# Optimization experiments

Hardware: AMD Instinct MI355X
Metric: run time of the kernel (lower is better)

Reference implementation:

```python
import jax, jax.numpy as jnp
import numpy as np

HEADS, DIM_HEAD, LANDMARKS, PINV_ITERS = 8, 64, 256, 6
DIM = 512
KERNEL = 33  # residual depthwise conv kernel size (lucidrains NystromAttention default)
EPS = 1e-5   # torch LayerNorm eps


def setup_inputs() -> dict:
    key = jax.random.key(0)
    ks = jax.random.split(key, 4)
    b, n = 4, 8192  # n divisible by LANDMARKS -> no padding branch
    w = lambda k, shape: jax.random.normal(k, shape, dtype=jnp.float32) * 0.02
    return {
        "x": jax.random.normal(ks[0], (b, n, DIM), dtype=jnp.float32),
        "ln_gamma": jnp.ones((DIM,), jnp.float32),
        "ln_beta": jnp.zeros((DIM,), jnp.float32),
        "w_qkv": w(ks[1], (DIM, 3 * HEADS * DIM_HEAD)),   # to_qkv, no bias
        "w_out": w(ks[2], (HEADS * DIM_HEAD, DIM)),
        "b_out": jnp.zeros((DIM,), jnp.float32),
        "res_kernel": w(ks[3], (HEADS, 1, KERNEL, 1)),    # Conv2d(heads, heads, (33,1), groups=heads)
    }


def _moore_penrose_pinv(a, iters):
    # iterative Moore-Penrose pseudoinverse (lucidrains)
    abs_a = jnp.abs(a)
    col = abs_a.sum(-1).max()  # global max, matching torch.max(col)
    row = abs_a.sum(-2).max()
    z = jnp.swapaxes(a, -1, -2) / (col * row)
    I = jnp.eye(a.shape[-1], dtype=a.dtype)
    for _ in range(iters):
        az = a @ z
        z = 0.25 * z @ (13.0 * I - az @ (15.0 * I - az @ (7.0 * I - az)))
    return z


def reference(x, ln_gamma, ln_beta, w_qkv, w_out, b_out, res_kernel):
    b, n, d = x.shape
    h, dh, m = HEADS, DIM_HEAD, LANDMARKS
    # --- LayerNorm ---
    mu = x.mean(-1, keepdims=True)
    var = ((x - mu) ** 2).mean(-1, keepdims=True)
    xn = (x - mu) * jax.lax.rsqrt(var + EPS) * ln_gamma + ln_beta
    # --- qkv projection ---
    qkv = xn @ w_qkv                                   # (b, n, 3*h*dh)
    q, k, v = jnp.split(qkv, 3, axis=-1)
    to_heads = lambda t: t.reshape(b, n, h, dh).transpose(0, 2, 1, 3)  # (b, h, n, dh)
    q, k, v = to_heads(q), to_heads(k), to_heads(v)
    q = q * (dh ** -0.5)
    # --- landmark pooling (mean over groups of l tokens) ---
    l = n // m
    q_l = q.reshape(b, h, m, l, dh).mean(3)            # (b, h, m, dh)
    k_l = k.reshape(b, h, m, l, dh).mean(3)
    # --- three similarity matrices + softmaxes ---
    attn1 = jax.nn.softmax(jnp.einsum('bhnd,bhmd->bhnm', q, k_l), axis=-1)    # (b,h,n,m)
    attn2 = jax.nn.softmax(jnp.einsum('bhid,bhjd->bhij', q_l, k_l), axis=-1)  # (b,h,m,m)
    attn3 = jax.nn.softmax(jnp.einsum('bhmd,bhnd->bhmn', q_l, k), axis=-1)    # (b,h,m,n)
    out = (attn1 @ _moore_penrose_pinv(attn2, PINV_ITERS)) @ (attn3 @ v)      # (b,h,n,dh)
    # --- depthwise residual conv over sequence dim (groups = heads) ---
    res = jax.lax.conv_general_dilated(
        v, res_kernel, window_strides=(1, 1),
        padding=((KERNEL // 2, KERNEL // 2), (0, 0)),
        dimension_numbers=('NCHW', 'OIHW', 'NCHW'),
        feature_group_count=h)
    out = out + res
    # --- merge heads, output projection, outer residual ---
    out = out.transpose(0, 2, 1, 3).reshape(b, n, h * dh)
    att = out @ w_out + b_out
    return x + att
```

## Files before the change

### kernel.cpp

```cpp
#include <hip/hip_runtime.h>
#include <math.h>

#define NB 4
#define NSEQ 8192
#define DMODEL 512
#define NHEADS 8
#define DHEAD 64
#define NLM 256
#define LTOK 32
#define NBH 32
#define KCONV 33
#define CH3 8

typedef unsigned short bf16_t;
typedef __attribute__((ext_vector_type(8))) short bf16x8;
typedef __attribute__((ext_vector_type(4))) float f32x4;

__device__ __forceinline__ float bf2f(bf16_t u) {
  return __uint_as_float(((unsigned)u) << 16);
}
__device__ __forceinline__ bf16_t f2bf(float f) {
  unsigned u = __float_as_uint(f);
  return (bf16_t)((u + 0x7fffu + ((u >> 16) & 1u)) >> 16);
}
__device__ __forceinline__ void bfpair(unsigned u, float& lo, float& hi) {
  lo = __uint_as_float(u << 16);
  hi = __uint_as_float(u & 0xffff0000u);
}
__device__ __forceinline__ void gload16(const bf16_t* g, bf16_t* l) {
  __builtin_amdgcn_global_load_lds(
      (const __attribute__((address_space(1))) unsigned int*)g,
      (__attribute__((address_space(3))) unsigned int*)l, 16, 0, 0);
}

__global__ __launch_bounds__(256) void ln_kernel(const float* __restrict__ x,
    const float* __restrict__ gamma, const float* __restrict__ beta,
    bf16_t* __restrict__ xn) {
  int row = blockIdx.x * 4 + (threadIdx.x >> 6);
  int lane = threadIdx.x & 63;
  const float4* xr = reinterpret_cast<const float4*>(x + (size_t)row * DMODEL);
  float4 a0 = xr[lane];
  float4 a1 = xr[lane + 64];
  float s  = a0.x + a0.y + a0.z + a0.w + a1.x + a1.y + a1.z + a1.w;
  float s2 = a0.x*a0.x + a0.y*a0.y + a0.z*a0.z + a0.w*a0.w
           + a1.x*a1.x + a1.y*a1.y + a1.z*a1.z + a1.w*a1.w;
  #pragma unroll
  for (int off = 32; off; off >>= 1) {
    s  += __shfl_down(s, off);
    s2 += __shfl_down(s2, off);
  }
  s = __shfl(s, 0); s2 = __shfl(s2, 0);
  float mu = s * (1.0f / DMODEL);
  float var = s2 * (1.0f / DMODEL) - mu * mu;
  float rs = rsqrtf(var + 1e-5f);
  const float4* g4 = reinterpret_cast<const float4*>(gamma);
  const float4* b4 = reinterpret_cast<const float4*>(beta);
  float4 g0 = g4[lane], g1 = g4[lane + 64];
  float4 bb0 = b4[lane], bb1 = b4[lane + 64];
  ushort4 o0, o1;
  o0.x = f2bf((a0.x - mu) * rs * g0.x + bb0.x);
  o0.y = f2bf((a0.y - mu) * rs * g0.y + bb0.y);
  o0.z = f2bf((a0.z - mu) * rs * g0.z + bb0.z);
  o0.w = f2bf((a0.w - mu) * rs * g0.w + bb0.w);
  o1.x = f2bf((a1.x - mu) * rs * g1.x + bb1.x);
  o1.y = f2bf((a1.y - mu) * rs * g1.y + bb1.y);
  o1.z = f2bf((a1.z - mu) * rs * g1.z + bb1.z);
  o1.w = f2bf((a1.w - mu) * rs * g1.w + bb1.w);
  ushort4* o = reinterpret_cast<ushort4*>(xn + (size_t)row * DMODEL);
  o[lane] = o0; o[lane + 64] = o1;
}

__global__ void castT2_kernel(const float* __restrict__ wqkv, const float* __restrict__ wout,
                              bf16_t* __restrict__ wqkvT, bf16_t* __restrict__ woutT) {
  int idx = blockIdx.x * 256 + threadIdx.x;
  if (idx < 786432) {
    int k = idx & 511, c = idx >> 9;
    float v = wqkv[(size_t)k * 1536 + c];
    if (c < 512) v *= 0.125f;
    wqkvT[idx] = f2bf(v);
  } else {
    int i = idx - 786432;
    int k = i & 511, c = i >> 9;
    woutT[i] = f2bf(wout[(size_t)k * 512 + c]);
  }
}

__global__ __launch_bounds__(256) void gemm_qkv_mfma(const bf16_t* __restrict__ A,
    const bf16_t* __restrict__ Bt, bf16_t* __restrict__ q, bf16_t* __restrict__ k,
    bf16_t* __restrict__ v) {
  __shared__ __align__(16) bf16_t As[128 * 32];
  __shared__ __align__(16) bf16_t Bs[128 * 32];
  int rowB = blockIdx.x * 128, colB = blockIdx.y * 128;
  int tid = threadIdx.x;
  int wave = tid >> 6, lane = tid & 63;
  int wr = (wave >> 1) * 64, wc = (wave & 1) * 64;
  int lrow = lane & 15, g = lane >> 4;
  f32x4 acc[4][4] = {};
  for (int k0 = 0; k0 < DMODEL; k0 += 32) {
    #pragma unroll
    for (int c = 0; c < 2; ++c) {
      int eb = wave * 1024 + c * 512;
      int e = eb + lane * 8;
      int r = e >> 5, cc = e & 31;
      gload16(A + (size_t)(rowB + r) * DMODEL + k0 + cc, &As[eb]);
      gload16(Bt + (size_t)(colB + r) * DMODEL + k0 + cc, &Bs[eb]);
    }
    __syncthreads();
    bf16x8 af[4], bf[4];
    #pragma unroll
    for (int m = 0; m < 4; ++m)
      af[m] = *reinterpret_cast<const bf16x8*>(&As[(wr + m * 16 + lrow) * 32 + g * 8]);
    #pragma unroll
    for (int n = 0; n < 4; ++n)
      bf[n] = *reinterpret_cast<const bf16x8*>(&Bs[(wc + n * 16 + lrow) * 32 + g * 8]);
    #pragma unroll
    for (int m = 0; m < 4; ++m)
      #pragma unroll
      for (int n = 0; n < 4; ++n)
        acc[m][n] = __builtin_amdgcn_mfma_f32_16x16x32_bf16(af[m], bf[n], acc[m][n], 0, 0, 0);
    __syncthreads();
  }
  #pragma unroll
  for (int m = 0; m < 4; ++m) {
    #pragma unroll
    for (int n = 0; n < 4; ++n) {
      int col = colB + wc + n * 16 + lrow;
      int which = col >> 9, hc = col & 511, h = hc >> 6, d = hc & 63;
      bf16_t* dst = (which == 0) ? q : (which == 1 ? k : v);
      #pragma unroll
      for (int r = 0; r < 4; ++r) {
        int row = rowB + wr + m * 16 + g * 4 + r;
        int b = row >> 13, nn = row & 8191;
        dst[((size_t)(b * NHEADS + h) * NSEQ + nn) * DHEAD + d] = f2bf(acc[m][n][r]);
      }
    }
  }
}

__global__ __launch_bounds__(256) void gemm_out_mfma(const bf16_t* __restrict__ A,
    const bf16_t* __restrict__ Bt, const float* __restrict__ bo,
    const float* __restrict__ x, float* __restrict__ y) {
  __shared__ __align__(16) bf16_t As[128 * 32];
  __shared__ __align__(16) bf16_t Bs[128 * 32];
  int rowB = blockIdx.x * 128, colB = blockIdx.y * 128;
  int tid = threadIdx.x;
  int wave = tid >> 6, lane = tid & 63;
  int wr = (wave >> 1) * 64, wc = (wave & 1) * 64;
  int lrow = lane & 15, g = lane >> 4;
  f32x4 acc[4][4] = {};
  for (int k0 = 0; k0 < DMODEL; k0 += 32) {
    #pragma unroll
    for (int c = 0; c < 2; ++c) {
      int eb = wave * 1024 + c * 512;
      int e = eb + lane * 8;
      int r = e >> 5, cc = e & 31;
      gload16(A + (size_t)(rowB + r) * DMODEL + k0 + cc, &As[eb]);
      gload16(Bt + (size_t)(colB + r) * DMODEL + k0 + cc, &Bs[eb]);
    }
    __syncthreads();
    bf16x8 af[4], bf[4];
    #pragma unroll
    for (int m = 0; m < 4; ++m)
      af[m] = *reinterpret_cast<const bf16x8*>(&As[(wr + m * 16 + lrow) * 32 + g * 8]);
    #pragma unroll
    for (int n = 0; n < 4; ++n)
      bf[n] = *reinterpret_cast<const bf16x8*>(&Bs[(wc + n * 16 + lrow) * 32 + g * 8]);
    #pragma unroll
    for (int n = 0; n < 4; ++n)
      #pragma unroll
      for (int m = 0; m < 4; ++m)
        acc[n][m] = __builtin_amdgcn_mfma_f32_16x16x32_bf16(bf[n], af[m], acc[n][m], 0, 0, 0);
    __syncthreads();
  }
  #pragma unroll
  for (int n = 0; n < 4; ++n) {
    int c0 = colB + wc + n * 16 + g * 4;
    float4 b4 = *reinterpret_cast<const float4*>(&bo[c0]);
    #pragma unroll
    for (int m = 0; m < 4; ++m) {
      int row = rowB + wr + m * 16 + lrow;
      size_t off = (size_t)row * DMODEL + c0;
      float4 xv = *reinterpret_cast<const float4*>(&x[off]);
      float4 o;
      o.x = xv.x + b4.x + acc[n][m][0];
      o.y = xv.y + b4.y + acc[n][m][1];
      o.z = xv.z + b4.z + acc[n][m][2];
      o.w = xv.w + b4.w + acc[n][m][3];
      *reinterpret_cast<float4*>(&y[off]) = o;
    }
  }
}

__global__ __launch_bounds__(256) void transpose64_kernel(const bf16_t* __restrict__ src,
    bf16_t* __restrict__ dst, int R) {
  __shared__ __align__(16) bf16_t T[64 * 64];
  int r0 = blockIdx.x * 64, bh = blockIdx.y;
  int tid = threadIdx.x;
  int jj = tid >> 2, part = tid & 3;
  const uint4* sr = reinterpret_cast<const uint4*>(
      src + ((size_t)bh * R + r0 + jj) * 64 + part * 16);
  uint4 a0 = sr[0], a1 = sr[1];
  int xr = (jj >> 3) & 7;
  int pg0 = (part * 2) ^ xr, pg1 = (part * 2 + 1) ^ xr;
  *reinterpret_cast<uint4*>(&T[jj * 64 + pg0 * 8]) = a0;
  *reinterpret_cast<uint4*>(&T[jj * 64 + pg1 * 8]) = a1;
  __syncthreads();
  int d = tid >> 2;
  unsigned ow[8];
  #pragma unroll
  for (int ee = 0; ee < 8; ++ee) {
    int n1 = part * 16 + ee * 2, n2 = n1 + 1;
    unsigned lo = T[n1 * 64 + (((d >> 3) ^ ((n1 >> 3) & 7)) * 8) + (d & 7)];
    unsigned hi = T[n2 * 64 + (((d >> 3) ^ ((n2 >> 3) & 7)) * 8) + (d & 7)];
    ow[ee] = lo | (hi << 16);
  }
  uint4* ot = reinterpret_cast<uint4*>(dst + ((size_t)bh * 64 + d) * R + r0 + part * 16);
  ot[0] = make_uint4(ow[0], ow[1], ow[2], ow[3]);
  ot[1] = make_uint4(ow[4], ow[5], ow[6], ow[7]);
}

__global__ void pool_kernel(const bf16_t* __restrict__ q, const bf16_t* __restrict__ k,
                            float* __restrict__ ql, float* __restrict__ kl,
                            bf16_t* __restrict__ qlb, bf16_t* __restrict__ klb) {
  int idx = blockIdx.x * 256 + threadIdx.x;
  const int half = NBH * NLM * DHEAD;
  const bf16_t* src = (idx < half) ? q : k;
  float* dst = (idx < half) ? ql : kl;
  bf16_t* dstb = (idx < half) ? qlb : klb;
  int i = (idx < half) ? idx : idx - half;
  int d = i & 63, m = (i >> 6) & 255, bh = i >> 14;
  const bf16_t* p = src + ((size_t)bh * NSEQ + m * LTOK) * DHEAD + d;
  float sum = 0.f;
  #pragma unroll
  for (int t = 0; t < LTOK; ++t) sum += bf2f(p[(size_t)t * DHEAD]);
  float r = sum * (1.0f / LTOK);
  dst[i] = r;
  dstb[i] = f2bf(r);
}

__global__ __launch_bounds__(256) void attn2_kernel(const float* __restrict__ ql,
    const float* __restrict__ kl, float* __restrict__ a2) {
  __shared__ float qs[64];
  __shared__ float red[256];
  int bh = blockIdx.y, i = blockIdx.x, t = threadIdx.x;
  if (t < 64) qs[t] = ql[((size_t)bh * NLM + i) * DHEAD + t];
  __syncthreads();
  const float* kr = kl + ((size_t)bh * NLM + t) * DHEAD;
  float s = 0.f;
  #pragma unroll
  for (int d = 0; d < 64; ++d) s += qs[d] * kr[d];
  red[t] = s; __syncthreads();
  for (int off = 128; off; off >>= 1) { if (t < off) red[t] = fmaxf(red[t], red[t + off]); __syncthreads(); }
  float mx = red[0]; __syncthreads();
  float p = expf(s - mx);
  red[t] = p; __syncthreads();
  for (int off = 128; off; off >>= 1) { if (t < off) red[t] += red[t + off]; __syncthreads(); }
  a2[((size_t)bh * NLM + i) * NLM + t] = p / red[0];
}

__global__ void zero2_kernel(unsigned int* __restrict__ scal) {
  if (threadIdx.x < 2) scal[threadIdx.x] = 0u;
}

__global__ void colrow_kernel(const float* __restrict__ a2, unsigned int* __restrict__ scal) {
  int bh = blockIdx.x & 31, mode = blockIdx.x >> 5;
  int t = threadIdx.x;
  const float* Ab = a2 + (size_t)bh * NLM * NLM;
  float sum = 0.f;
  if (mode == 0) { for (int j = 0; j < NLM; ++j) sum += fabsf(Ab[(size_t)t * NLM + j]); }
  else           { for (int i2 = 0; i2 < NLM; ++i2) sum += fabsf(Ab[(size_t)i2 * NLM + t]); }
  __shared__ float red[256];
  red[t] = sum; __syncthreads();
  for (int off = 128; off; off >>= 1) { if (t < off) red[t] = fmaxf(red[t], red[t + off]); __syncthreads(); }
  if (t == 0) atomicMax(&scal[mode], __float_as_uint(red[0]));
}

__global__ void zinit_kernel(const float* __restrict__ a2, const unsigned int* __restrict__ scal,
                             bf16_t* __restrict__ zb, bf16_t* __restrict__ a2b) {
  int idx = blockIdx.x * 256 + threadIdx.x;
  float inv = 1.0f / (__uint_as_float(scal[0]) * __uint_as_float(scal[1]));
  int j = idx & 255, i = (idx >> 8) & 255, bh = idx >> 16;
  zb[idx] = f2bf(a2[((size_t)bh * NLM + j) * NLM + i] * inv);
  a2b[idx] = f2bf(a2[idx]);
}

__global__ __launch_bounds__(256) void matmul256_b2b(bf16_t* __restrict__ C,
    const bf16_t* __restrict__ A, const bf16_t* __restrict__ Bm, float s, float alpha) {
  __shared__ __align__(16) bf16_t Ah[64][72];
  __shared__ __align__(16) bf16_t Bh[64][72];
  int bh = blockIdx.y;
  const bf16_t* Ab = A + (size_t)bh * NLM * NLM;
  const bf16_t* Bb = Bm + (size_t)bh * NLM * NLM;
  bf16_t* Cb = C + (size_t)bh * NLM * NLM;
  int rowB = (blockIdx.x >> 2) * 64, colB = (blockIdx.x & 3) * 64;
  int tid = threadIdx.x, w = tid >> 6, lane = tid & 63, tx = lane & 15, g = lane >> 4;
  int jj = tid >> 2, part = tid & 3;
  f32x4 acc[4] = {};
  for (int k0 = 0; k0 < NLM; k0 += 64) {
    {
      const uint4* ar = reinterpret_cast<const uint4*>(
          Ab + (size_t)(rowB + jj) * NLM + k0 + part * 16);
      *reinterpret_cast<uint4*>(&Ah[jj][part * 16]) = ar[0];
      *reinterpret_cast<uint4*>(&Ah[jj][part * 16 + 8]) = ar[1];
      const uint4* br = reinterpret_cast<const uint4*>(
          Bb + (size_t)(k0 + jj) * NLM + colB + part * 16);
      uint4 b0 = br[0], b1 = br[1];
      int d0 = part * 16;
      Bh[d0+ 0][jj] = (bf16_t)(b0.x & 0xffffu); Bh[d0+ 1][jj] = (bf16_t)(b0.x >> 16);
      Bh[d0+ 2][jj] = (bf16_t)(b0.y & 0xffffu); Bh[d0+ 3][jj] = (bf16_t)(b0.y >> 16);
      Bh[d0+ 4][jj] = (bf16_t)(b0.z & 0xffffu); Bh[d0+ 5][jj] = (bf16_t)(b0.z >> 16);
      Bh[d0+ 6][jj] = (bf16_t)(b0.w & 0xffffu); Bh[d0+ 7][jj] = (bf16_t)(b0.w >> 16);
      Bh[d0+ 8][jj] = (bf16_t)(b1.x & 0xffffu); Bh[d0+ 9][jj] = (bf16_t)(b1.x >> 16);
      Bh[d0+10][jj] = (bf16_t)(b1.y & 0xffffu); Bh[d0+11][jj] = (bf16_t)(b1.y >> 16);
      Bh[d0+12][jj] = (bf16_t)(b1.z & 0xffffu); Bh[d0+13][jj] = (bf16_t)(b1.z >> 16);
      Bh[d0+14][jj] = (bf16_t)(b1.w & 0xffffu); Bh[d0+15][jj] = (bf16_t)(b1.w >> 16);
    }
    __syncthreads();
    #pragma unroll
    for (int ks = 0; ks < 2; ++ks) {
      bf16x8 ah = *reinterpret_cast<const bf16x8*>(&Ah[w * 16 + tx][g * 8 + 32 * ks]);
      #pragma unroll
      for (int tn = 0; tn < 4; ++tn) {
        bf16x8 bhf = *reinterpret_cast<const bf16x8*>(&Bh[tn * 16 + tx][g * 8 + 32 * ks]);
        acc[tn] = __builtin_amdgcn_mfma_f32_16x16x32_bf16(bhf, ah, acc[tn], 0, 0, 0);
      }
    }
    __syncthreads();
  }
  int rr = rowB + w * 16 + tx;
  #pragma unroll
  for (int tn = 0; tn < 4; ++tn) {
    int c0 = colB + tn * 16 + g * 4;
    size_t off = (size_t)rr * NLM + c0;
    float a0 = 0.f, a1 = 0.f, a2v = 0.f, a3 = 0.f;
    if (s != 0.0f) {
      ushort4 av = *reinterpret_cast<const ushort4*>(&Ab[off]);
      a0 = bf2f(av.x); a1 = bf2f(av.y); a2v = bf2f(av.z); a3 = bf2f(av.w);
    }
    ushort4 o;
    o.x = f2bf(alpha * (s * a0 - acc[tn][0]));
    o.y = f2bf(alpha * (s * a1 - acc[tn][1]));
    o.z = f2bf(alpha * (s * a2v - acc[tn][2]));
    o.w = f2bf(alpha * (s * a3 - acc[tn][3]));
    *reinterpret_cast<ushort4*>(&Cb[off]) = o;
  }
}

__global__ __launch_bounds__(256) void matmul256_b2f(float* __restrict__ C,
    const bf16_t* __restrict__ A, const bf16_t* __restrict__ Bm, float s, float alpha) {
  __shared__ __align__(16) bf16_t Ah[64][72];
  __shared__ __align__(16) bf16_t Bh[64][72];
  int bh = blockIdx.y;
  const bf16_t* Ab = A + (size_t)bh * NLM * NLM;
  const bf16_t* Bb = Bm + (size_t)bh * NLM * NLM;
  float* Cb = C + (size_t)bh * NLM * NLM;
  int rowB = (blockIdx.x >> 2) * 64, colB = (blockIdx.x & 3) * 64;
  int tid = threadIdx.x, w = tid >> 6, lane = tid & 63, tx = lane & 15, g = lane >> 4;
  int jj = tid >> 2, part = tid & 3;
  f32x4 acc[4] = {};
  for (int k0 = 0; k0 < NLM; k0 += 64) {
    {
      const uint4* ar = reinterpret_cast<const uint4*>(
          Ab + (size_t)(rowB + jj) * NLM + k0 + part * 16);
      *reinterpret_cast<uint4*>(&Ah[jj][part * 16]) = ar[0];
      *reinterpret_cast<uint4*>(&Ah[jj][part * 16 + 8]) = ar[1];
      const uint4* br = reinterpret_cast<const uint4*>(
          Bb + (size_t)(k0 + jj) * NLM + colB + part * 16);
      uint4 b0 = br[0], b1 = br[1];
      int d0 = part * 16;
      Bh[d0+ 0][jj] = (bf16_t)(b0.x & 0xffffu); Bh[d0+ 1][jj] = (bf16_t)(b0.x >> 16);
      Bh[d0+ 2][jj] = (bf16_t)(b0.y & 0xffffu); Bh[d0+ 3][jj] = (bf16_t)(b0.y >> 16);
      Bh[d0+ 4][jj] = (bf16_t)(b0.z & 0xffffu); Bh[d0+ 5][jj] = (bf16_t)(b0.z >> 16);
      Bh[d0+ 6][jj] = (bf16_t)(b0.w & 0xffffu); Bh[d0+ 7][jj] = (bf16_t)(b0.w >> 16);
      Bh[d0+ 8][jj] = (bf16_t)(b1.x & 0xffffu); Bh[d0+ 9][jj] = (bf16_t)(b1.x >> 16);
      Bh[d0+10][jj] = (bf16_t)(b1.y & 0xffffu); Bh[d0+11][jj] = (bf16_t)(b1.y >> 16);
      Bh[d0+12][jj] = (bf16_t)(b1.z & 0xffffu); Bh[d0+13][jj] = (bf16_t)(b1.z >> 16);
      Bh[d0+14][jj] = (bf16_t)(b1.w & 0xffffu); Bh[d0+15][jj] = (bf16_t)(b1.w >> 16);
    }
    __syncthreads();
    #pragma unroll
    for (int ks = 0; ks < 2; ++ks) {
      bf16x8 ah = *reinterpret_cast<const bf16x8*>(&Ah[w * 16 + tx][g * 8 + 32 * ks]);
      #pragma unroll
      for (int tn = 0; tn < 4; ++tn) {
        bf16x8 bhf = *reinterpret_cast<const bf16x8*>(&Bh[tn * 16 + tx][g * 8 + 32 * ks]);
        acc[tn] = __builtin_amdgcn_mfma_f32_16x16x32_bf16(bhf, ah, acc[tn], 0, 0, 0);
      }
    }
    __syncthreads();
  }
  int rr = rowB + w * 16 + tx;
  #pragma unroll
  for (int tn = 0; tn < 4; ++tn) {
    int c0 = colB + tn * 16 + g * 4;
    size_t off = (size_t)rr * NLM + c0;
    float a0 = 0.f, a1 = 0.f, a2v = 0.f, a3 = 0.f;
    if (s != 0.0f) {
      ushort4 av = *reinterpret_cast<const ushort4*>(&Ab[off]);
      a0 = bf2f(av.x); a1 = bf2f(av.y); a2v = bf2f(av.z); a3 = bf2f(av.w);
    }
    float4 o;
    o.x = alpha * (s * a0 - acc[tn][0]);
    o.y = alpha * (s * a1 - acc[tn][1]);
    o.z = alpha * (s * a2v - acc[tn][2]);
    o.w = alpha * (s * a3 - acc[tn][3]);
    *reinterpret_cast<float4*>(&Cb[off]) = o;
  }
}

__global__ __launch_bounds__(256) void attn3v_mfma(const bf16_t* __restrict__ qlb,
    const bf16_t* __restrict__ k, const bf16_t* __restrict__ vT,
    float* __restrict__ Wpart, float* __restrict__ mlpart) {
  __shared__ __align__(16) bf16_t Qs[64][72];
  __shared__ __align__(16) bf16_t Ks[64][72];
  __shared__ __align__(16) bf16_t Vt[64][72];
  __shared__ __align__(16) bf16_t Ps[64][72];
  int chunk = blockIdx.x, lmt = blockIdx.y, bh = blockIdx.z;
  int tid = threadIdx.x;
  int w = tid >> 6, lane = tid & 63;
  int tx = lane & 15, g = lane >> 4;
  int lm0 = lmt * 64;
  int jj = tid >> 2, part = tid & 3;
  {
    const uint4* qr = reinterpret_cast<const uint4*>(
        qlb + ((size_t)bh * NLM + lm0 + jj) * DHEAD + part * 16);
    *reinterpret_cast<uint4*>(&Qs[jj][part * 16]) = qr[0];
    *reinterpret_cast<uint4*>(&Qs[jj][part * 16 + 8]) = qr[1];
  }
  f32x4 oacc[4] = {};
  float lreg[4] = {0.f, 0.f, 0.f, 0.f};
  const bf16_t* kb = k + (size_t)bh * NSEQ * DHEAD;
  const bf16_t* vtb = vT + (size_t)bh * DHEAD * NSEQ + (size_t)jj * NSEQ;
  __syncthreads();
  for (int it = 0; it < NSEQ / (CH3 * 64); ++it) {
    int n0 = chunk * (NSEQ / CH3) + it * 64;
    {
      const uint4* kr = reinterpret_cast<const uint4*>(kb + (size_t)(n0 + jj) * DHEAD + part * 16);
      *reinterpret_cast<uint4*>(&Ks[jj][part * 16]) = kr[0];
      *reinterpret_cast<uint4*>(&Ks[jj][part * 16 + 8]) = kr[1];
      const uint4* vr = reinterpret_cast<const uint4*>(vtb + n0 + part * 16);
      *reinterpret_cast<uint4*>(&Vt[jj][part * 16]) = vr[0];
      *reinterpret_cast<uint4*>(&Vt[jj][part * 16 + 8]) = vr[1];
// ... 172 lines not shown
    *reinterpret_cast<ushort4*>(
        &outp[((size_t)(b * NSEQ + n)) * DMODEL + h * DHEAD + td * 16 + g * 4]) = o;
  }
}

__global__ void conv_kernel(const bf16_t* __restrict__ v, const float* __restrict__ rk,
                            bf16_t* __restrict__ outp) {
  int t = blockIdx.x * 256 + threadIdx.x;
  int d8 = t & 7, h = (t >> 3) & 7, n = (t >> 6) & 8191, b = t >> 19;
  const bf16_t* vb = v + ((size_t)(b * NHEADS + h) * NSEQ) * DHEAD + d8 * 8;
  const float* wk = rk + h * KCONV;
  float a0 = 0.f, a1 = 0.f, a2 = 0.f, a3 = 0.f, a4 = 0.f, a5 = 0.f, a6 = 0.f, a7 = 0.f;
  #pragma unroll
  for (int tp = 0; tp < KCONV; ++tp) {
    int nn = n + tp - 16;
    if (nn < 0 || nn >= NSEQ) continue;
    uint4 vv = *reinterpret_cast<const uint4*>(vb + (size_t)nn * DHEAD);
    float wgt = wk[tp];
    float lo, hi;
    bfpair(vv.x, lo, hi); a0 += lo * wgt; a1 += hi * wgt;
    bfpair(vv.y, lo, hi); a2 += lo * wgt; a3 += hi * wgt;
    bfpair(vv.z, lo, hi); a4 += lo * wgt; a5 += hi * wgt;
    bfpair(vv.w, lo, hi); a6 += lo * wgt; a7 += hi * wgt;
  }
  size_t ob = ((size_t)(b * NSEQ + n)) * DMODEL + h * DHEAD + d8 * 8;
  uint4 ov = *reinterpret_cast<uint4*>(outp + ob);
  float lo, hi;
  uint4 nv;
  bfpair(ov.x, lo, hi); nv.x = ((unsigned)f2bf(lo + a0)) | (((unsigned)f2bf(hi + a1)) << 16);
  bfpair(ov.y, lo, hi); nv.y = ((unsigned)f2bf(lo + a2)) | (((unsigned)f2bf(hi + a3)) << 16);
  bfpair(ov.z, lo, hi); nv.z = ((unsigned)f2bf(lo + a4)) | (((unsigned)f2bf(hi + a5)) << 16);
  bfpair(ov.w, lo, hi); nv.w = ((unsigned)f2bf(lo + a6)) | (((unsigned)f2bf(hi + a7)) << 16);
  *reinterpret_cast<uint4*>(outp + ob) = nv;
}

extern "C" void kernel_launch(void* const* d_in, const int* in_sizes, int n_in,
                              void* d_out, int out_size, void* d_ws, size_t ws_size,
                              hipStream_t stream) {
  const float* x     = (const float*)d_in[0];
  const float* gamma = (const float*)d_in[1];
  const float* beta  = (const float*)d_in[2];
  const float* wqkv  = (const float*)d_in[3];
  const float* wout  = (const float*)d_in[4];
  const float* bout  = (const float*)d_in[5];
  const float* rk    = (const float*)d_in[6];
  float* y = (float*)d_out;

  char* wsb = (char*)d_ws;
  bf16_t* xn = (bf16_t*)(wsb);
  bf16_t* q  = (bf16_t*)(wsb + 33554432ull);
  bf16_t* k  = (bf16_t*)(wsb + 67108864ull);
  bf16_t* v  = (bf16_t*)(wsb + 100663296ull);
  float* a2f = (float*)(wsb + 134217728ull);
  bf16_t* a2b = (bf16_t*)(wsb + 150994944ull);
  bf16_t* zb  = (bf16_t*)(wsb + 155189248ull);
  bf16_t* azb = (bf16_t*)(wsb + 159383552ull);
  bf16_t* t1b = (bf16_t*)(wsb + 163577856ull);
  bf16_t* t2b = (bf16_t*)(wsb + 167772160ull);
  float* zf  = (float*)(wsb + 150994944ull);
  float* ql  = (float*)(wsb + 176160768ull);
  float* kl  = (float*)(wsb + 178257920ull);
  float* Wm  = (float*)(wsb + 180355072ull);
  bf16_t* Ub = (bf16_t*)(wsb + 182452224ull);
  unsigned int* scal = (unsigned int*)(wsb + 184549376ull);
  bf16_t* wqkvT = (bf16_t*)(wsb + 182452224ull);
  bf16_t* woutT = (bf16_t*)(wsb + 184549440ull);
  bf16_t* qlb = (bf16_t*)(wsb + 185073728ull);
  bf16_t* klb = (bf16_t*)(wsb + 186122304ull);
  bf16_t* Ut  = (bf16_t*)(wsb + 187170880ull);

  bf16_t* vT = xn;
  float* Wpart  = a2f;
  float* mlpart = (float*)(wsb + 167772160ull);
  bf16_t* out_pre = (bf16_t*)(wsb + 134217728ull);

  castT2_kernel<<<4096, 256, 0, stream>>>(wqkv, wout, wqkvT, woutT);
  ln_kernel<<<8192, 256, 0, stream>>>(x, gamma, beta, xn);
  gemm_qkv_mfma<<<dim3(256, 12), 256, 0, stream>>>(xn, wqkvT, q, k, v);
  transpose64_kernel<<<dim3(128, 32), 256, 0, stream>>>(v, vT, NSEQ);
  pool_kernel<<<4096, 256, 0, stream>>>(q, k, ql, kl, qlb, klb);
  attn2_kernel<<<dim3(256, 32), 256, 0, stream>>>(ql, kl, a2f);
  zero2_kernel<<<1, 64, 0, stream>>>(scal);
  colrow_kernel<<<64, 256, 0, stream>>>(a2f, scal);
  zinit_kernel<<<8192, 256, 0, stream>>>(a2f, scal, zb, a2b);

  bf16_t *pzb = zb, *pt2b = t2b;
  for (int it = 0; it < 5; ++it) {
    matmul256_b2b<<<dim3(16, 32), 256, 0, stream>>>(azb, a2b, pzb, 0.f, -1.f);
    matmul256_b2b<<<dim3(16, 32), 256, 0, stream>>>(pt2b, azb, azb, 7.f, 1.f);
    matmul256_b2b<<<dim3(16, 32), 256, 0, stream>>>(t1b, azb, pt2b, 15.f, 1.f);
    matmul256_b2b<<<dim3(16, 32), 256, 0, stream>>>(pt2b, pzb, t1b, 13.f, 0.25f);
    bf16_t* tmp = pzb; pzb = pt2b; pt2b = tmp;
  }
  matmul256_b2b<<<dim3(16, 32), 256, 0, stream>>>(azb, a2b, pzb, 0.f, -1.f);
  matmul256_b2b<<<dim3(16, 32), 256, 0, stream>>>(pt2b, azb, azb, 7.f, 1.f);
  matmul256_b2b<<<dim3(16, 32), 256, 0, stream>>>(t1b, azb, pt2b, 15.f, 1.f);
  matmul256_b2f<<<dim3(16, 32), 256, 0, stream>>>(zf, pzb, t1b, 13.f, 0.25f);

  attn3v_mfma<<<dim3(CH3, 4, 32), 256, 0, stream>>>(qlb, k, vT, Wpart, mlpart);
  attn3v_combine<<<2048, 256, 0, stream>>>(Wpart, mlpart, Wm);
  zw_kernel<<<2048, 256, 0, stream>>>(zf, Wm, Ub);
  transpose64_kernel<<<dim3(4, 32), 256, 0, stream>>>(Ub, Ut, NLM);
  attn1_mfma<<<dim3(128, 32), 256, 0, stream>>>(q, klb, Ut, out_pre);
  conv_kernel<<<8192, 256, 0, stream>>>(v, rk, out_pre);
  gemm_out_mfma<<<dim3(256, 4), 256, 0, stream>>>(out_pre, woutT, bout, x, y);
}
```

Measured before the change: 654.3 us.

## Widen GEMM K-steps, stage full K in pinv matmuls, fold scalar zeroing

The QKV and output GEMMs now load two 32-wide K slices per iteration into separate LDS buffers. This halves the number of barrier-separated loop trips. The 256x256 pseudoinverse matmuls stage the whole A row-panel and the transposed B column-panel (all K=256) into LDS once, then run eight MFMA k-steps with no inner syncs. The separate kernel that zeroes the col/row max scalars is removed and its work folded into the weight-cast kernel, saving one launch. The cost is more LDS per block in the pinv matmuls (about 67 KB), which can lower occupancy, and a bank-conflict-prone transposed scatter into LDS.

```diff
diff --git a/kernel.cpp b/kernel.cpp
--- a/kernel.cpp
+++ b/kernel.cpp
@@ -71,8 +71,10 @@
 }
 
 __global__ void castT2_kernel(const float* __restrict__ wqkv, const float* __restrict__ wout,
-                              bf16_t* __restrict__ wqkvT, bf16_t* __restrict__ woutT) {
+                              bf16_t* __restrict__ wqkvT, bf16_t* __restrict__ woutT,
+                              unsigned int* __restrict__ scal) {
   int idx = blockIdx.x * 256 + threadIdx.x;
+  if (idx < 2) scal[idx] = 0u;
   if (idx < 786432) {
     int k = idx & 511, c = idx >> 9;
     float v = wqkv[(size_t)k * 1536 + c];
@@ -88,36 +90,45 @@
 __global__ __launch_bounds__(256) void gemm_qkv_mfma(const bf16_t* __restrict__ A,
     const bf16_t* __restrict__ Bt, bf16_t* __restrict__ q, bf16_t* __restrict__ k,
     bf16_t* __restrict__ v) {
-  __shared__ __align__(16) bf16_t As[128 * 32];
-  __shared__ __align__(16) bf16_t Bs[128 * 32];
+  __shared__ __align__(16) bf16_t As0[128 * 32];
+  __shared__ __align__(16) bf16_t As1[128 * 32];
+  __shared__ __align__(16) bf16_t Bs0[128 * 32];
+  __shared__ __align__(16) bf16_t Bs1[128 * 32];
   int rowB = blockIdx.x * 128, colB = blockIdx.y * 128;
   int tid = threadIdx.x;
   int wave = tid >> 6, lane = tid & 63;
   int wr = (wave >> 1) * 64, wc = (wave & 1) * 64;
   int lrow = lane & 15, g = lane >> 4;
   f32x4 acc[4][4] = {};
-  for (int k0 = 0; k0 < DMODEL; k0 += 32) {
+  for (int k0 = 0; k0 < DMODEL; k0 += 64) {
     #pragma unroll
     for (int c = 0; c < 2; ++c) {
       int eb = wave * 1024 + c * 512;
       int e = eb + lane * 8;
       int r = e >> 5, cc = e & 31;
-      gload16(A + (size_t)(rowB + r) * DMODEL + k0 + cc, &As[eb]);
-      gload16(Bt + (size_t)(colB + r) * DMODEL + k0 + cc, &Bs[eb]);
-    }
-    __syncthreads();
-    bf16x8 af[4], bf[4];
-    #pragma unroll
-    for (int m = 0; m < 4; ++m)
-      af[m] = *reinterpret_cast<const bf16x8*>(&As[(wr + m * 16 + lrow) * 32 + g * 8]);
-    #pragma unroll
-    for (int n = 0; n < 4; ++n)
-      bf[n] = *reinterpret_cast<const bf16x8*>(&Bs[(wc + n * 16 + lrow) * 32 + g * 8]);
-    #pragma unroll
-    for (int m = 0; m < 4; ++m)
+      gload16(A + (size_t)(rowB + r) * DMODEL + k0 + cc, &As0[eb]);
+      gload16(A + (size_t)(rowB + r) * DMODEL + k0 + 32 + cc, &As1[eb]);
+      gload16(Bt + (size_t)(colB + r) * DMODEL + k0 + cc, &Bs0[eb]);
+      gload16(Bt + (size_t)(colB + r) * DMODEL + k0 + 32 + cc, &Bs1[eb]);
+    }
+    __syncthreads();
+    #pragma unroll
+    for (int ks = 0; ks < 2; ++ks) {
+      const bf16_t* Ab2 = ks ? As1 : As0;
+      const bf16_t* Bb2 = ks ? Bs1 : Bs0;
+      bf16x8 af[4], bf[4];
+      #pragma unroll
+      for (int m = 0; m < 4; ++m)
+        af[m] = *reinterpret_cast<const bf16x8*>(&Ab2[(wr + m * 16 + lrow) * 32 + g * 8]);
       #pragma unroll
       for (int n = 0; n < 4; ++n)
-        acc[m][n] = __builtin_amdgcn_mfma_f32_16x16x32_bf16(af[m], bf[n], acc[m][n], 0, 0, 0);
+        bf[n] = *reinterpret_cast<const bf16x8*>(&Bb2[(wc + n * 16 + lrow) * 32 + g * 8]);
+      #pragma unroll
+      for (int m = 0; m < 4; ++m)
+        #pragma unroll
+        for (int n = 0; n < 4; ++n)
+          acc[m][n] = __builtin_amdgcn_mfma_f32_16x16x32_bf16(af[m], bf[n], acc[m][n], 0, 0, 0);
+    }
     __syncthreads();
   }
   #pragma unroll
@@ -140,36 +151,45 @@
 __global__ __launch_bounds__(256) void gemm_out_mfma(const bf16_t* __restrict__ A,
     const bf16_t* __restrict__ Bt, const float* __restrict__ bo,
     const float* __restrict__ x, float* __restrict__ y) {
-  __shared__ __align__(16) bf16_t As[128 * 32];
-  __shared__ __align__(16) bf16_t Bs[128 * 32];
+  __shared__ __align__(16) bf16_t As0[128 * 32];
+  __shared__ __align__(16) bf16_t As1[128 * 32];
+  __shared__ __align__(16) bf16_t Bs0[128 * 32];
+  __shared__ __align__(16) bf16_t Bs1[128 * 32];
   int rowB = blockIdx.x * 128, colB = blockIdx.y * 128;
   int tid = threadIdx.x;
   int wave = tid >> 6, lane = tid & 63;
   int wr = (wave >> 1) * 64, wc = (wave & 1) * 64;
   int lrow = lane & 15, g = lane >> 4;
   f32x4 acc[4][4] = {};
-  for (int k0 = 0; k0 < DMODEL; k0 += 32) {
+  for (int k0 = 0; k0 < DMODEL; k0 += 64) {
     #pragma unroll
     for (int c = 0; c < 2; ++c) {
       int eb = wave * 1024 + c * 512;
       int e = eb + lane * 8;
       int r = e >> 5, cc = e & 31;
-      gload16(A + (size_t)(rowB + r) * DMODEL + k0 + cc, &As[eb]);
-      gload16(Bt + (size_t)(colB + r) * DMODEL + k0 + cc, &Bs[eb]);
-    }
-    __syncthreads();
-    bf16x8 af[4], bf[4];
-    #pragma unroll
-    for (int m = 0; m < 4; ++m)
-      af[m] = *reinterpret_cast<const bf16x8*>(&As[(wr + m * 16 + lrow) * 32 + g * 8]);
-    #pragma unroll
-    for (int n = 0; n < 4; ++n)
-      bf[n] = *reinterpret_cast<const bf16x8*>(&Bs[(wc + n * 16 + lrow) * 32 + g * 8]);
-    #pragma unroll
-    for (int n = 0; n < 4; ++n)
+      gload16(A + (size_t)(rowB + r) * DMODEL + k0 + cc, &As0[eb]);
+      gload16(A + (size_t)(rowB + r) * DMODEL + k0 + 32 + cc, &As1[eb]);
+      gload16(Bt + (size_t)(colB + r) * DMODEL + k0 + cc, &Bs0[eb]);
+      gload16(Bt + (size_t)(colB + r) * DMODEL + k0 + 32 + cc, &Bs1[eb]);
+    }
+    __syncthreads();
+    #pragma unroll
+    for (int ks = 0; ks < 2; ++ks) {
+      const bf16_t* Ab2 = ks ? As1 : As0;
+      const bf16_t* Bb2 = ks ? Bs1 : Bs0;
+      bf16x8 af[4], bf[4];
       #pragma unroll
       for (int m = 0; m < 4; ++m)
-        acc[n][m] = __builtin_amdgcn_mfma_f32_16x16x32_bf16(bf[n], af[m], acc[n][m], 0, 0, 0);
+        af[m] = *reinterpret_cast<const bf16x8*>(&Ab2[(wr + m * 16 + lrow) * 32 + g * 8]);
+      #pragma unroll
+      for (int n = 0; n < 4; ++n)
+        bf[n] = *reinterpret_cast<const bf16x8*>(&Bb2[(wc + n * 16 + lrow) * 32 + g * 8]);
+      #pragma unroll
+      for (int n = 0; n < 4; ++n)
+        #pragma unroll
+        for (int m = 0; m < 4; ++m)
+          acc[n][m] = __builtin_amdgcn_mfma_f32_16x16x32_bf16(bf[n], af[m], acc[n][m], 0, 0, 0);
+    }
     __syncthreads();
   }
   #pragma unroll
@@ -258,10 +278,6 @@
   a2[((size_t)bh * NLM + i) * NLM + t] = p / red[0];
 }
 
-__global__ void zero2_kernel(unsigned int* __restrict__ scal) {
-  if (threadIdx.x < 2) scal[threadIdx.x] = 0u;
-}
-
 __global__ void colrow_kernel(const float* __restrict__ a2, unsigned int* __restrict__ scal) {
   int bh = blockIdx.x & 31, mode = blockIdx.x >> 5;
   int t = threadIdx.x;
@@ -286,46 +302,48 @@
 
 __global__ __launch_bounds__(256) void matmul256_b2b(bf16_t* __restrict__ C,
     const bf16_t* __restrict__ A, const bf16_t* __restrict__ Bm, float s, float alpha) {
-  __shared__ __align__(16) bf16_t Ah[64][72];
-  __shared__ __align__(16) bf16_t Bh[64][72];
+  __shared__ __align__(16) bf16_t Ah[64][264];
+  __shared__ __align__(16) bf16_t Btl[64][264];
   int bh = blockIdx.y;
   const bf16_t* Ab = A + (size_t)bh * NLM * NLM;
   const bf16_t* Bb = Bm + (size_t)bh * NLM * NLM;
   bf16_t* Cb = C + (size_t)bh * NLM * NLM;
   int rowB = (blockIdx.x >> 2) * 64, colB = (blockIdx.x & 3) * 64;
   int tid = threadIdx.x, w = tid >> 6, lane = tid & 63, tx = lane & 15, g = lane >> 4;
-  int jj = tid >> 2, part = tid & 3;
+  {
+    int row = tid >> 2, seg = tid & 3;
+    const uint4* ar = reinterpret_cast<const uint4*>(
+        Ab + (size_t)(rowB + row) * NLM + seg * 64);
+    uint4* aw = reinterpret_cast<uint4*>(&Ah[row][seg * 64]);
+    #pragma unroll
+    for (int i = 0; i < 8; ++i) aw[i] = ar[i];
+    #pragma unroll
+    for (int kc = 0; kc < 4; ++kc) {
+      int kk = row + kc * 64;
+      const uint4* br = reinterpret_cast<const uint4*>(
+          Bb + (size_t)kk * NLM + colB + seg * 16);
+      uint4 b0 = br[0], b1 = br[1];
+      int d0 = seg * 16;
+      Btl[d0+ 0][kk] = (bf16_t)(b0.x & 0xffffu); Btl[d0+ 1][kk] = (bf16_t)(b0.x >> 16);
+      Btl[d0+ 2][kk] = (bf16_t)(b0.y & 0xffffu); Btl[d0+ 3][kk] = (bf16_t)(b0.y >> 16);
+      Btl[d0+ 4][kk] = (bf16_t)(b0.z & 0xffffu); Btl[d0+ 5][kk] = (bf16_t)(b0.z >> 16);
+      Btl[d0+ 6][kk] = (bf16_t)(b0.w & 0xffffu); Btl[d0+ 7][kk] = (bf16_t)(b0.w >> 16);
+      Btl[d0+ 8][kk] = (bf16_t)(b1.x & 0xffffu); Btl[d0+ 9][kk] = (bf16_t)(b1.x >> 16);
+      Btl[d0+10][kk] = (bf16_t)(b1.y & 0xffffu); Btl[d0+11][kk] = (bf16_t)(b1.y >> 16);
+      Btl[d0+12][kk] = (bf16_t)(b1.z & 0xffffu); Btl[d0+13][kk] = (bf16_t)(b1.z >> 16);
+      Btl[d0+14][kk] = (bf16_t)(b1.w & 0xffffu); Btl[d0+15][kk] = (bf16_t)(b1.w >> 16);
+    }
+  }
+  __syncthreads();
   f32x4 acc[4] = {};
-  for (int k0 = 0; k0 < NLM; k0 += 64) {
-    {
-      const uint4* ar = reinterpret_cast<const uint4*>(
-          Ab + (size_t)(rowB + jj) * NLM + k0 + part * 16);
-      *reinterpret_cast<uint4*>(&Ah[jj][part * 16]) = ar[0];
-      *reinterpret_cast<uint4*>(&Ah[jj][part * 16 + 8]) = ar[1];
-      const uint4* br = reinterpret_cast<const uint4*>(
-          Bb + (size_t)(k0 + jj) * NLM + colB + part * 16);
-      uint4 b0 = br[0], b1 = br[1];
-      int d0 = part * 16;
-      Bh[d0+ 0][jj] = (bf16_t)(b0.x & 0xffffu); Bh[d0+ 1][jj] = (bf16_t)(b0.x >> 16);
-      Bh[d0+ 2][jj] = (bf16_t)(b0.y & 0xffffu); Bh[d0+ 3][jj] = (bf16_t)(b0.y >> 16);
-      Bh[d0+ 4][jj] = (bf16_t)(b0.z & 0xffffu); Bh[d0+ 5][jj] = (bf16_t)(b0.z >> 16);
-      Bh[d0+ 6][jj] = (bf16_t)(b0.w & 0xffffu); Bh[d0+ 7][jj] = (bf16_t)(b0.w >> 16);
-      Bh[d0+ 8][jj] = (bf16_t)(b1.x & 0xffffu); Bh[d0+ 9][jj] = (bf16_t)(b1.x >> 16);
-      Bh[d0+10][jj] = (bf16_t)(b1.y & 0xffffu); Bh[d0+11][jj] = (bf16_t)(b1.y >> 16);
-      Bh[d0+12][jj] = (bf16_t)(b1.z & 0xffffu); Bh[d0+13][jj] = (bf16_t)(b1.z >> 16);
-      Bh[d0+14][jj] = (bf16_t)(b1.w & 0xffffu); Bh[d0+15][jj] = (bf16_t)(b1.w >> 16);
-    }
-    __syncthreads();
-    #pragma unroll
-    for (int ks = 0; ks < 2; ++ks) {
-      bf16x8 ah = *reinterpret_cast<const bf16x8*>(&Ah[w * 16 + tx][g * 8 + 32 * ks]);
-      #pragma unroll
-      for (int tn = 0; tn < 4; ++tn) {
-        bf16x8 bhf = *reinterpret_cast<const bf16x8*>(&Bh[tn * 16 + tx][g * 8 + 32 * ks]);
-        acc[tn] = __builtin_amdgcn_mfma_f32_16x16x32_bf16(bhf, ah, acc[tn], 0, 0, 0);
-      }
-    }
-    __syncthreads();
+  #pragma unroll
+  for (int ks = 0; ks < 8; ++ks) {
+    bf16x8 ah = *reinterpret_cast<const bf16x8*>(&Ah[w * 16 + tx][ks * 32 + g * 8]);
+    #pragma unroll
+    for (int tn = 0; tn < 4; ++tn) {
+      bf16x8 bt = *reinterpret_cast<const bf16x8*>(&Btl[tn * 16 + tx][ks * 32 + g * 8]);
+      acc[tn] = __builtin_amdgcn_mfma_f32_16x16x32_bf16(bt, ah, acc[tn], 0, 0, 0);
+    }
   }
   int rr = rowB + w * 16 + tx;
   #pragma unroll
@@ -348,46 +366,48 @@
 
 __global__ __launch_bounds__(256) void matmul256_b2f(float* __restrict__ C,
     const bf16_t* __restrict__ A, const bf16_t* __restrict__ Bm, float s, float alpha) {
-  __shared__ __align__(16) bf16_t Ah[64][72];
-  __shared__ __align__(16) bf16_t Bh[64][72];
+  __shared__ __align__(16) bf16_t Ah[64][264];
+  __shared__ __align__(16) bf16_t Btl[64][264];
   int bh = blockIdx.y;
   const bf16_t* Ab = A + (size_t)bh * NLM * NLM;
   const bf16_t* Bb = Bm + (size_t)bh * NLM * NLM;
   float* Cb = C + (size_t)bh * NLM * NLM;
   int rowB = (blockIdx.x >> 2) * 64, colB = (blockIdx.x & 3) * 64;
   int tid = threadIdx.x, w = tid >> 6, lane = tid & 63, tx = lane & 15, g = lane >> 4;
-  int jj = tid >> 2, part = tid & 3;
+  {
+    int row = tid >> 2, seg = tid & 3;
+    const uint4* ar = reinterpret_cast<const uint4*>(
+        Ab + (size_t)(rowB + row) * NLM + seg * 64);
+    uint4* aw = reinterpret_cast<uint4*>(&Ah[row][seg * 64]);
+    #pragma unroll
+    for (int i = 0; i < 8; ++i) aw[i] = ar[i];
+    #pragma unroll
+    for (int kc = 0; kc < 4; ++kc) {
+      int kk = row + kc * 64;
+      const uint4* br = reinterpret_cast<const uint4*>(
+          Bb + (size_t)kk * NLM + colB + seg * 16);
+      uint4 b0 = br[0], b1 = br[1];
+      int d0 = seg * 16;
+      Btl[d0+ 0][kk] = (bf16_t)(b0.x & 0xffffu); Btl[d0+ 1][kk] = (bf16_t)(b0.x >> 16);
+      Btl[d0+ 2][kk] = (bf16_t)(b0.y & 0xffffu); Btl[d0+ 3][kk] = (bf16_t)(b0.y >> 16);
+      Btl[d0+ 4][kk] = (bf16_t)(b0.z & 0xffffu); Btl[d0+ 5][kk] = (bf16_t)(b0.z >> 16);
+      Btl[d0+ 6][kk] = (bf16_t)(b0.w & 0xffffu); Btl[d0+ 7][kk] = (bf16_t)(b0.w >> 16);
+      Btl[d0+ 8][kk] = (bf16_t)(b1.x & 0xffffu); Btl[d0+ 9][kk] = (bf16_t)(b1.x >> 16);
+      Btl[d0+10][kk] = (bf16_t)(b1.y & 0xffffu); Btl[d0+11][kk] = (bf16_t)(b1.y >> 16);
+      Btl[d0+12][kk] = (bf16_t)(b1.z & 0xffffu); Btl[d0+13][kk] = (bf16_t)(b1.z >> 16);
+      Btl[d0+14][kk] = (bf16_t)(b1.w & 0xffffu); Btl[d0+15][kk] = (bf16_t)(b1.w >> 16);
+    }
+  }
+  __syncthreads();
   f32x4 acc[4] = {};
-  for (int k0 = 0; k0 < NLM; k0 += 64) {
-    {
-      const uint4* ar = reinterpret_cast<const uint4*>(
-          Ab + (size_t)(rowB + jj) * NLM + k0 + part * 16);
-      *reinterpret_cast<uint4*>(&Ah[jj][part * 16]) = ar[0];
-      *reinterpret_cast<uint4*>(&Ah[jj][part * 16 + 8]) = ar[1];
-      const uint4* br = reinterpret_cast<const uint4*>(
-          Bb + (size_t)(k0 + jj) * NLM + colB + part * 16);
-      uint4 b0 = br[0], b1 = br[1];
-      int d0 = part * 16;
-      Bh[d0+ 0][jj] = (bf16_t)(b0.x & 0xffffu); Bh[d0+ 1][jj] = (bf16_t)(b0.x >> 16);
-      Bh[d0+ 2][jj] = (bf16_t)(b0.y & 0xffffu); Bh[d0+ 3][jj] = (bf16_t)(b0.y >> 16);
-      Bh[d0+ 4][jj] = (bf16_t)(b0.z & 0xffffu); Bh[d0+ 5][jj] = (bf16_t)(b0.z >> 16);
-      Bh[d0+ 6][jj] = (bf16_t)(b0.w & 0xffffu); Bh[d0+ 7][jj] = (bf16_t)(b0.w >> 16);
-      Bh[d0+ 8][jj] = (bf16_t)(b1.x & 0xffffu); Bh[d0+ 9][jj] = (bf16_t)(b1.x >> 16);
-      Bh[d0+10][jj] = (bf16_t)(b1.y & 0xffffu); Bh[d0+11][jj] = (bf16_t)(b1.y >> 16);
-      Bh[d0+12][jj] = (bf16_t)(b1.z & 0xffffu); Bh[d0+13][jj] = (bf16_t)(b1.z >> 16);
-      Bh[d0+14][jj] = (bf16_t)(b1.w & 0xffffu); Bh[d0+15][jj] = (bf16_t)(b1.w >> 16);
-    }
-    __syncthreads();
-    #pragma unroll
-    for (int ks = 0; ks < 2; ++ks) {
-      bf16x8 ah = *reinterpret_cast<const bf16x8*>(&Ah[w * 16 + tx][g * 8 + 32 * ks]);
-      #pragma unroll
-      for (int tn = 0; tn < 4; ++tn) {
-        bf16x8 bhf = *reinterpret_cast<const bf16x8*>(&Bh[tn * 16 + tx][g * 8 + 32 * ks]);
-        acc[tn] = __builtin_amdgcn_mfma_f32_16x16x32_bf16(bhf, ah, acc[tn], 0, 0, 0);
-      }
-    }
-    __syncthreads();
+  #pragma unroll
+  for (int ks = 0; ks < 8; ++ks) {
+    bf16x8 ah = *reinterpret_cast<const bf16x8*>(&Ah[w * 16 + tx][ks * 32 + g * 8]);
+    #pragma unroll
+    for (int tn = 0; tn < 4; ++tn) {
+      bf16x8 bt = *reinterpret_cast<const bf16x8*>(&Btl[tn * 16 + tx][ks * 32 + g * 8]);
+      acc[tn] = __builtin_amdgcn_mfma_f32_16x16x32_bf16(bt, ah, acc[tn], 0, 0, 0);
+    }
   }
   int rr = rowB + w * 16 + tx;
   #pragma unroll
@@ -688,13 +708,12 @@
   float* mlpart = (float*)(wsb + 167772160ull);
   bf16_t* out_pre = (bf16_t*)(wsb + 134217728ull);
 
-  castT2_kernel<<<4096, 256, 0, stream>>>(wqkv, wout, wqkvT, woutT);
+  castT2_kernel<<<4096, 256, 0, stream>>>(wqkv, wout, wqkvT, woutT, scal);
   ln_kernel<<<8192, 256, 0, stream>>>(x, gamma, beta, xn);
   gemm_qkv_mfma<<<dim3(256, 12), 256, 0, stream>>>(xn, wqkvT, q, k, v);
   transpose64_kernel<<<dim3(128, 32), 256, 0, stream>>>(v, vT, NSEQ);
   pool_kernel<<<4096, 256, 0, stream>>>(q, k, ql, kl, qlb, klb);
   attn2_kernel<<<dim3(256, 32), 256, 0, stream>>>(ql, kl, a2f);
-  zero2_kernel<<<1, 64, 0, stream>>>(scal);
   colrow_kernel<<<64, 256, 0, stream>>>(a2f, scal);
   zinit_kernel<<<8192, 256, 0, stream>>>(a2f, scal, zb, a2b);
 
```

Result: slower. 677.6 us (+3.6%).

## Restructure pinv iteration to track A·Z product and batch two matmuls per launch

Applied to the files above, without the earlier changes.

The Newton-Schulz pseudoinverse loop now carries Y = -(A·Z) across iterations, updating it alongside Z by computing A·Znew as Y·M in one batched launch with two z-slices. This removes the separate A·Z matmul each iteration and cuts launch count from four to three per iteration. The zero-scalar init is folded into the weight-cast kernel, dropping one tiny launch. Carrying Y in bf16 rather than recomputing it from A and Z may let rounding error drift across iterations.

```diff
diff --git a/kernel.cpp b/kernel.cpp
--- a/kernel.cpp
+++ b/kernel.cpp
@@ -71,8 +71,10 @@
 }
 
 __global__ void castT2_kernel(const float* __restrict__ wqkv, const float* __restrict__ wout,
-                              bf16_t* __restrict__ wqkvT, bf16_t* __restrict__ woutT) {
+                              bf16_t* __restrict__ wqkvT, bf16_t* __restrict__ woutT,
+                              unsigned int* __restrict__ scal) {
   int idx = blockIdx.x * 256 + threadIdx.x;
+  if (idx < 2) scal[idx] = 0u;
   if (idx < 786432) {
     int k = idx & 511, c = idx >> 9;
     float v = wqkv[(size_t)k * 1536 + c];
@@ -256,10 +258,6 @@
   red[t] = p; __syncthreads();
   for (int off = 128; off; off >>= 1) { if (t < off) red[t] += red[t + off]; __syncthreads(); }
   a2[((size_t)bh * NLM + i) * NLM + t] = p / red[0];
-}
-
-__global__ void zero2_kernel(unsigned int* __restrict__ scal) {
-  if (threadIdx.x < 2) scal[threadIdx.x] = 0u;
 }
 
 __global__ void colrow_kernel(const float* __restrict__ a2, unsigned int* __restrict__ scal) {
@@ -346,6 +344,69 @@
   }
 }
 
+__global__ __launch_bounds__(256) void matmul256_b2b2(
+    bf16_t* __restrict__ C0, const bf16_t* __restrict__ A0,
+    bf16_t* __restrict__ C1, const bf16_t* __restrict__ A1,
+    const bf16_t* __restrict__ Bm, float s, float alpha) {
+  __shared__ __align__(16) bf16_t Ah[64][72];
+  __shared__ __align__(16) bf16_t Bh[64][72];
+  int bh = blockIdx.y;
+  const bf16_t* A = (blockIdx.z == 0) ? A0 : A1;
+  bf16_t* C = (blockIdx.z == 0) ? C0 : C1;
+  const bf16_t* Ab = A + (size_t)bh * NLM * NLM;
+  const bf16_t* Bb = Bm + (size_t)bh * NLM * NLM;
+  bf16_t* Cb = C + (size_t)bh * NLM * NLM;
+  int rowB = (blockIdx.x >> 2) * 64, colB = (blockIdx.x & 3) * 64;
+  int tid = threadIdx.x, w = tid >> 6, lane = tid & 63, tx = lane & 15, g = lane >> 4;
+  int jj = tid >> 2, part = tid & 3;
+  f32x4 acc[4] = {};
+  for (int k0 = 0; k0 < NLM; k0 += 64) {
+    {
+      const uint4* ar = reinterpret_cast<const uint4*>(
+          Ab + (size_t)(rowB + jj) * NLM + k0 + part * 16);
+      *reinterpret_cast<uint4*>(&Ah[jj][part * 16]) = ar[0];
+      *reinterpret_cast<uint4*>(&Ah[jj][part * 16 + 8]) = ar[1];
+      const uint4* br = reinterpret_cast<const uint4*>(
+          Bb + (size_t)(k0 + jj) * NLM + colB + part * 16);
+      uint4 b0 = br[0], b1 = br[1];
+      int d0 = part * 16;
+      Bh[d0+ 0][jj] = (bf16_t)(b0.x & 0xffffu); Bh[d0+ 1][jj] = (bf16_t)(b0.x >> 16);
+      Bh[d0+ 2][jj] = (bf16_t)(b0.y & 0xffffu); Bh[d0+ 3][jj] = (bf16_t)(b0.y >> 16);
+      Bh[d0+ 4][jj] = (bf16_t)(b0.z & 0xffffu); Bh[d0+ 5][jj] = (bf16_t)(b0.z >> 16);
+      Bh[d0+ 6][jj] = (bf16_t)(b0.w & 0xffffu); Bh[d0+ 7][jj] = (bf16_t)(b0.w >> 16);
+      Bh[d0+ 8][jj] = (bf16_t)(b1.x & 0xffffu); Bh[d0+ 9][jj] = (bf16_t)(b1.x >> 16);
+      Bh[d0+10][jj] = (bf16_t)(b1.y & 0xffffu); Bh[d0+11][jj] = (bf16_t)(b1.y >> 16);
+      Bh[d0+12][jj] = (bf16_t)(b1.z & 0xffffu); Bh[d0+13][jj] = (bf16_t)(b1.z >> 16);
+      Bh[d0+14][jj] = (bf16_t)(b1.w & 0xffffu); Bh[d0+15][jj] = (bf16_t)(b1.w >> 16);
+    }
+    __syncthreads();
+    #pragma unroll
+    for (int ks = 0; ks < 2; ++ks) {
+      bf16x8 ah = *reinterpret_cast<const bf16x8*>(&Ah[w * 16 + tx][g * 8 + 32 * ks]);
+      #pragma unroll
+      for (int tn = 0; tn < 4; ++tn) {
+        bf16x8 bhf = *reinterpret_cast<const bf16x8*>(&Bh[tn * 16 + tx][g * 8 + 32 * ks]);
+        acc[tn] = __builtin_amdgcn_mfma_f32_16x16x32_bf16(bhf, ah, acc[tn], 0, 0, 0);
+      }
+    }
+    __syncthreads();
+  }
+  int rr = rowB + w * 16 + tx;
+  #pragma unroll
+  for (int tn = 0; tn < 4; ++tn) {
+    int c0 = colB + tn * 16 + g * 4;
+    size_t off = (size_t)rr * NLM + c0;
+    ushort4 av = *reinterpret_cast<const ushort4*>(&Ab[off]);
+    float a0 = bf2f(av.x), a1 = bf2f(av.y), a2v = bf2f(av.z), a3 = bf2f(av.w);
+    ushort4 o;
+    o.x = f2bf(alpha * (s * a0 - acc[tn][0]));
+    o.y = f2bf(alpha * (s * a1 - acc[tn][1]));
+    o.z = f2bf(alpha * (s * a2v - acc[tn][2]));
+    o.w = f2bf(alpha * (s * a3 - acc[tn][3]));
+    *reinterpret_cast<ushort4*>(&Cb[off]) = o;
+  }
+}
+
 __global__ __launch_bounds__(256) void matmul256_b2f(float* __restrict__ C,
     const bf16_t* __restrict__ A, const bf16_t* __restrict__ Bm, float s, float alpha) {
   __shared__ __align__(16) bf16_t Ah[64][72];
@@ -666,11 +727,13 @@
   bf16_t* k  = (bf16_t*)(wsb + 67108864ull);
   bf16_t* v  = (bf16_t*)(wsb + 100663296ull);
   float* a2f = (float*)(wsb + 134217728ull);
+  bf16_t* M2b = (bf16_t*)(wsb + 134217728ull);
+  bf16_t* M3b = (bf16_t*)(wsb + 138412032ull);
   bf16_t* a2b = (bf16_t*)(wsb + 150994944ull);
-  bf16_t* zb  = (bf16_t*)(wsb + 155189248ull);
-  bf16_t* azb = (bf16_t*)(wsb + 159383552ull);
-  bf16_t* t1b = (bf16_t*)(wsb + 163577856ull);
-  bf16_t* t2b = (bf16_t*)(wsb + 167772160ull);
+  bf16_t* zA  = (bf16_t*)(wsb + 155189248ull);
+  bf16_t* zB  = (bf16_t*)(wsb + 159383552ull);
+  bf16_t* YA  = (bf16_t*)(wsb + 163577856ull);
+  bf16_t* YB  = (bf16_t*)(wsb + 167772160ull);
   float* zf  = (float*)(wsb + 150994944ull);
   float* ql  = (float*)(wsb + 176160768ull);
   float* kl  = (float*)(wsb + 178257920ull);
@@ -684,32 +747,32 @@
   bf16_t* Ut  = (bf16_t*)(wsb + 187170880ull);
 
   bf16_t* vT = xn;
-  float* Wpart  = a2f;
+  float* Wpart  = (float*)(wsb + 134217728ull);
   float* mlpart = (float*)(wsb + 167772160ull);
   bf16_t* out_pre = (bf16_t*)(wsb + 134217728ull);
 
-  castT2_kernel<<<4096, 256, 0, stream>>>(wqkv, wout, wqkvT, woutT);
+  castT2_kernel<<<4096, 256, 0, stream>>>(wqkv, wout, wqkvT, woutT, scal);
   ln_kernel<<<8192, 256, 0, stream>>>(x, gamma, beta, xn);
   gemm_qkv_mfma<<<dim3(256, 12), 256, 0, stream>>>(xn, wqkvT, q, k, v);
   transpose64_kernel<<<dim3(128, 32), 256, 0, stream>>>(v, vT, NSEQ);
   pool_kernel<<<4096, 256, 0, stream>>>(q, k, ql, kl, qlb, klb);
   attn2_kernel<<<dim3(256, 32), 256, 0, stream>>>(ql, kl, a2f);
-  zero2_kernel<<<1, 64, 0, stream>>>(scal);
   colrow_kernel<<<64, 256, 0, stream>>>(a2f, scal);
-  zinit_kernel<<<8192, 256, 0, stream>>>(a2f, scal, zb, a2b);
-
-  bf16_t *pzb = zb, *pt2b = t2b;
+  zinit_kernel<<<8192, 256, 0, stream>>>(a2f, scal, zA, a2b);
+
+  matmul256_b2b<<<dim3(16, 32), 256, 0, stream>>>(YA, a2b, zA, 0.f, -1.f);
+  bf16_t *zc = zA, *zn = zB, *Yc = YA, *Yn = YB;
   for (int it = 0; it < 5; ++it) {
-    matmul256_b2b<<<dim3(16, 32), 256, 0, stream>>>(azb, a2b, pzb, 0.f, -1.f);
-    matmul256_b2b<<<dim3(16, 32), 256, 0, stream>>>(pt2b, azb, azb, 7.f, 1.f);
-    matmul256_b2b<<<dim3(16, 32), 256, 0, stream>>>(t1b, azb, pt2b, 15.f, 1.f);
-    matmul256_b2b<<<dim3(16, 32), 256, 0, stream>>>(pt2b, pzb, t1b, 13.f, 0.25f);
-    bf16_t* tmp = pzb; pzb = pt2b; pt2b = tmp;
-  }
-  matmul256_b2b<<<dim3(16, 32), 256, 0, stream>>>(azb, a2b, pzb, 0.f, -1.f);
-  matmul256_b2b<<<dim3(16, 32), 256, 0, stream>>>(pt2b, azb, azb, 7.f, 1.f);
-  matmul256_b2b<<<dim3(16, 32), 256, 0, stream>>>(t1b, azb, pt2b, 15.f, 1.f);
-  matmul256_b2f<<<dim3(16, 32), 256, 0, stream>>>(zf, pzb, t1b, 13.f, 0.25f);
+    matmul256_b2b<<<dim3(16, 32), 256, 0, stream>>>(M2b, Yc, Yc, 7.f, 1.f);
+    matmul256_b2b<<<dim3(16, 32), 256, 0, stream>>>(M3b, Yc, M2b, 15.f, 1.f);
+    matmul256_b2b2<<<dim3(16, 32, 2), 256, 0, stream>>>(zn, zc, Yn, Yc, M3b, 13.f, 0.25f);
+    bf16_t* t;
+    t = zc; zc = zn; zn = t;
+    t = Yc; Yc = Yn; Yn = t;
+  }
+  matmul256_b2b<<<dim3(16, 32), 256, 0, stream>>>(M2b, Yc, Yc, 7.f, 1.f);
+  matmul256_b2b<<<dim3(16, 32), 256, 0, stream>>>(M3b, Yc, M2b, 15.f, 1.f);
+  matmul256_b2f<<<dim3(16, 32), 256, 0, stream>>>(zf, zc, M3b, 13.f, 0.25f);
 
   attn3v_mfma<<<dim3(CH3, 4, 32), 256, 0, stream>>>(qlb, k, vT, Wpart, mlpart);
   attn3v_combine<<<2048, 256, 0, stream>>>(Wpart, mlpart, Wm);
```

New measurement: 632.5 us. 1.03x faster.
